# Kernel optimization log

Hardware: AMD Instinct MI355X
Metric: run time of the kernel (lower is better)

## Reference

```python
import jax, jax.numpy as jnp
import numpy as np

IMG = 1536
STRIDES = [8, 16, 32, 64, 128]
SCALES = np.array([2.0 ** 0, 2.0 ** (1.0 / 3.0), 2.0 ** (2.0 / 3.0)])
RATIOS = np.array([0.5, 1.0, 2.0])
THRESHOLD = 0.5
IOU_THRESHOLD = 0.5
N_KEEP = 1000  # fixed candidate budget for jit-compatible NMS


def make_anchors():
    """Multi-level RetinaNet-style anchors in (x1, y1, x2, y2), [A, 4]."""
    all_boxes = []
    for s in STRIDES:
        base = 4.0 * s
        fs = IMG // s
        areas = (base * SCALES) ** 2
        ws, hs = [], []
        for r in RATIOS:
            ws.append(np.sqrt(areas / r))
            hs.append(np.sqrt(areas * r))
        ws = np.concatenate(ws)  # [9]
        hs = np.concatenate(hs)
        cx = (np.arange(fs) + 0.5) * s
        cy = (np.arange(fs) + 0.5) * s
        cxg, cyg = np.meshgrid(cx, cy)
        cxg = cxg.reshape(-1, 1)
        cyg = cyg.reshape(-1, 1)
        boxes = np.stack([cxg - ws / 2, cyg - hs / 2, cxg + ws / 2, cyg + hs / 2], axis=-1)
        all_boxes.append(boxes.reshape(-1, 4))
    return np.concatenate(all_boxes, axis=0).astype(np.float32)


def setup_inputs() -> dict:
    key = jax.random.key(0)
    k1, k2 = jax.random.split(key)
    anchors = jnp.asarray(make_anchors())  # [441936, 4]
    A = anchors.shape[0]
    cla = jax.random.uniform(k1, (1, A, 80), dtype=jnp.float32)  # sigmoid-like class scores
    reg = 0.1 * jax.random.normal(k2, (1, A, 4), dtype=jnp.float32)  # box deltas
    return {"cla": cla, "reg": reg, "anchors": anchors, "height": IMG, "width": IMG}


def decode_box(anchors, deltas):
    wa = anchors[:, 2] - anchors[:, 0]
    ha = anchors[:, 3] - anchors[:, 1]
    cxa = anchors[:, 0] + 0.5 * wa
    cya = anchors[:, 1] + 0.5 * ha
    cx = cxa + deltas[:, 0] * wa
    cy = cya + deltas[:, 1] * ha
    w = wa * jnp.exp(deltas[:, 2])
    h = ha * jnp.exp(deltas[:, 3])
    return jnp.stack([cx - 0.5 * w, cy - 0.5 * h, cx + 0.5 * w, cy + 0.5 * h], axis=-1)


def iou_matrix(b):
    x1 = jnp.maximum(b[:, None, 0], b[None, :, 0])
    y1 = jnp.maximum(b[:, None, 1], b[None, :, 1])
    x2 = jnp.minimum(b[:, None, 2], b[None, :, 2])
    y2 = jnp.minimum(b[:, None, 3], b[None, :, 3])
    inter = jnp.clip(x2 - x1, 0.0) * jnp.clip(y2 - y1, 0.0)
    area = jnp.clip(b[:, 2] - b[:, 0], 0.0) * jnp.clip(b[:, 3] - b[:, 1], 0.0)
    union = area[:, None] + area[None, :] - inter
    return inter / jnp.maximum(union, 1e-8)


def reference(cla, reg, anchors, height, width):
    # decode + clip (clipbox)
    boxes = decode_box(anchors, reg[0])  # [A, 4]
    boxes = jnp.stack([
        jnp.clip(boxes[:, 0], 0.0, width - 1.0),
        jnp.clip(boxes[:, 1], 0.0, height - 1.0),
        jnp.clip(boxes[:, 2], 0.0, width - 1.0),
        jnp.clip(boxes[:, 3], 0.0, height - 1.0),
    ], axis=-1)
    # per-anchor best class score (torch.max over dim=2)
    scores_all = jnp.max(cla[0], axis=1)  # [A]
    # fixed-size candidate set replaces data-dependent boolean masking
    top_scores, idx = jax.lax.top_k(scores_all, N_KEEP)
    cand_boxes = boxes[idx]            # [N, 4]
    cand_cla = cla[0][idx]             # [N, C]
    valid = top_scores > THRESHOLD     # score thresholding
    iou = iou_matrix(cand_boxes)       # [N, N]

    def body(i, keep):
        suppressed = jnp.any(keep & (iou[i] > IOU_THRESHOLD))
        return keep.at[i].set(valid[i] & ~suppressed)

    keep = jax.lax.fori_loop(0, N_KEEP, body, jnp.zeros((N_KEEP,), dtype=bool))

    nms_scores = jnp.where(keep, jnp.max(cand_cla, axis=1), 0.0)
    nms_class = jnp.where(keep, jnp.argmax(cand_cla, axis=1), -1)
    nms_boxes = jnp.where(keep[:, None], cand_boxes, 0.0)
    return nms_scores, nms_class, nms_boxes
```

## Files before the change

### kernel.cpp

```cpp
#include <hip/hip_runtime.h>
#include <stdint.h>


#define NK 1000
#define CAP 2048
#define NCLS 80
#define NW 16
typedef unsigned long long ull;

static inline __device__ unsigned fkey(float f) {
  unsigned u = __float_as_uint(f);
  return (u & 0x80000000u) ? ~u : (u | 0x80000000u);
}
static inline __device__ float fkey_inv(unsigned k) {
  unsigned u = (k & 0x80000000u) ? (k & 0x7fffffffu) : ~k;
  return __uint_as_float(u);
}

__device__ __forceinline__ void scan_select(const unsigned* __restrict__ gh, int nbins,
                                            unsigned k, unsigned* s_sum, unsigned* s_res,
                                            unsigned& digit, unsigned& cum_above) {
  int t = threadIdx.x;
  int chunk = nbins >> 8;
  if (chunk < 1) chunk = 1;
  int base = t * chunk;
  unsigned s = 0;
  for (int b = 0; b < chunk; ++b) s += gh[base + b];
  s_sum[t] = s;
  __syncthreads();
  unsigned ca = 0;
  for (int u = t + 1; u < 256; ++u) ca += s_sum[u];
  if (ca < k && ca + s >= k) {
    unsigned cum = ca;
    for (int b = chunk - 1; b >= 0; --b) {
      unsigned c = gh[base + b];
      if (cum + c >= k) { s_res[0] = (unsigned)(base + b); s_res[1] = cum; break; }
      cum += c;
    }
  }
  __syncthreads();
  digit = s_res[0];
  cum_above = s_res[1];
  __syncthreads();
}

__global__ __launch_bounds__(256) void k_score(const float* __restrict__ cla,
                                               unsigned* __restrict__ keys,
                                               unsigned* __restrict__ hist0,
                                               uint4* __restrict__ zreg, int nz4,
                                               int A) {
  __shared__ unsigned lh[4096];
  int t = threadIdx.x;
  {
    const uint4 z = make_uint4(0u, 0u, 0u, 0u);
    int stride = gridDim.x * 256;
    for (int i = blockIdx.x * 256 + t; i < nz4; i += stride) zreg[i] = z;
  }
  for (int i = t; i < 4096; i += 256) lh[i] = 0u;
  __syncthreads();
  const int lane = t & 63, wib = t >> 6;
  const int gwave = blockIdx.x * 4 + wib, nwaves = gridDim.x * 4;
  const int q = lane >> 2, sub = lane & 3;
  const int ntask = (A + 15) >> 4;
  for (int task = gwave; task < ntask; task += nwaves) {
    int a = task * 16 + q;
    float m = -3.402823466e38f;
    if (a < A) {
      const float4* p = (const float4*)(cla + (size_t)a * NCLS);
#pragma unroll
      for (int j = 0; j < 5; ++j) {
        float4 v = p[sub + j * 4];
        m = fmaxf(m, fmaxf(fmaxf(v.x, v.y), fmaxf(v.z, v.w)));
      }
    }
    m = fmaxf(m, __shfl_xor(m, 1, 64));
    m = fmaxf(m, __shfl_xor(m, 2, 64));
    if (sub == 0 && a < A) {
      unsigned key = fkey(m);
      keys[a] = key;
      atomicAdd(&lh[key >> 20], 1u);
    }
  }
  __syncthreads();
  for (int i = t; i < 4096; i += 256) {
    unsigned c = lh[i];
    if (c) atomicAdd(&hist0[i], c);
  }
}

__global__ __launch_bounds__(256) void k_hist1(const unsigned* __restrict__ keys,
                                               const unsigned* __restrict__ hist0,
                                               unsigned* __restrict__ leaf,
                                               unsigned* __restrict__ summary, int A) {
  __shared__ unsigned lh[4096];
  __shared__ unsigned s_sum[256];
  __shared__ unsigned s_res[2];
  int t = threadIdx.x;
  unsigned d0, ca;
  scan_select(hist0, 4096, NK, s_sum, s_res, d0, ca);
  for (int i = t; i < 4096; i += 256) lh[i] = 0u;
  __syncthreads();
  int tid = blockIdx.x * 256 + t, nthr = gridDim.x * 256;
  for (int a = tid; a < A; a += nthr) {
    unsigned key = keys[a];
    if ((key >> 20) == d0) {
      unsigned low = key & 0xFFFFFu;
      atomicAdd(&leaf[low], 1u);
      atomicAdd(&lh[low >> 8], 1u);
    }
  }
  __syncthreads();
  for (int i = t; i < 4096; i += 256) {
    unsigned c = lh[i];
    if (c) atomicAdd(&summary[i], c);
  }
}

__global__ __launch_bounds__(256) void k_gather(const unsigned* __restrict__ keys,
                                                const unsigned* __restrict__ hist0,
                                                const unsigned* __restrict__ leaf,
                                                const unsigned* __restrict__ summary,
                                                unsigned* __restrict__ meta,
                                                ull* __restrict__ cand_keys, int A) {
  __shared__ unsigned s_sum[256];
  __shared__ unsigned s_res[2];
  __shared__ ull lbuf[1024];
  __shared__ unsigned lcnt;
  __shared__ unsigned gbase;
  int t = threadIdx.x;
  unsigned k_rem = NK, d0, g, b, ca;
  scan_select(hist0, 4096, k_rem, s_sum, s_res, d0, ca);
  k_rem -= ca;
  scan_select(summary, 4096, k_rem, s_sum, s_res, g, ca);
  k_rem -= ca;
  scan_select(leaf + (size_t)g * 256, 256, k_rem, s_sum, s_res, b, ca);
  const unsigned T = (d0 << 20) | (g << 8) | b;
  if (t == 0) lcnt = 0u;
  __syncthreads();
  int tid = blockIdx.x * 256 + t, nthr = gridDim.x * 256;
  for (int a = tid; a < A; a += nthr) {
    unsigned key = keys[a];
    if (key >= T) {
      unsigned pos = atomicAdd(&lcnt, 1u);
      if (pos < 1024)
        lbuf[pos] = ((ull)key << 32) | (ull)(~(unsigned)a);
    }
  }
  __syncthreads();
  if (t == 0) gbase = (lcnt > 0) ? atomicAdd(&meta[0], lcnt) : 0u;
  __syncthreads();
  unsigned n = lcnt < 1024u ? lcnt : 1024u;
  for (unsigned i = t; i < n; i += 256) {
    unsigned pos = gbase + i;
    if (pos < CAP) cand_keys[pos] = lbuf[i];
  }
}

__global__ __launch_bounds__(256) void k_rankdec(
    const float* __restrict__ cla, const float* __restrict__ reg,
    const float* __restrict__ anchors, const int* __restrict__ hp,
    const int* __restrict__ wp, const ull* __restrict__ cand_keys,
    float4* __restrict__ cand_box, float* __restrict__ cand_area,
    float* __restrict__ cand_score, int* __restrict__ cand_cls,
    int* __restrict__ cand_valid) {
  __shared__ ull skeys[CAP];
  int t = threadIdx.x;
  for (int i = t; i < CAP; i += 256) skeys[i] = cand_keys[i];
  __syncthreads();
  int c = blockIdx.x * 256 + t;
  ull ck = skeys[c];
  if (ck == 0ull) return;
  unsigned cnt = 0;
  const ulonglong2* sk2 = (const ulonglong2*)skeys;
#pragma unroll 4
  for (int j = 0; j < CAP / 2; ++j) {
    ulonglong2 v = sk2[j];
    cnt += (v.x > ck) ? 1u : 0u;
    cnt += (v.y > ck) ? 1u : 0u;
  }
  if (cnt >= NK) return;
  int rank = (int)cnt;
  unsigned a = ~(unsigned)(ck & 0xFFFFFFFFull);
  float score = fkey_inv((unsigned)(ck >> 32));
  float W1 = (float)wp[0] - 1.0f;
  float H1 = (float)hp[0] - 1.0f;
  float4 dd = ((const float4*)reg)[a];
  float4 an = ((const float4*)anchors)[a];
  float wa = an.z - an.x, ha = an.w - an.y;
  float cxa = an.x + 0.5f * wa, cya = an.y + 0.5f * ha;
  float cx = cxa + dd.x * wa, cy = cya + dd.y * ha;
  float w = wa * expf(dd.z), h = ha * expf(dd.w);
  float x1 = fminf(fmaxf(cx - 0.5f * w, 0.0f), W1);
  float y1 = fminf(fmaxf(cy - 0.5f * h, 0.0f), H1);
  float x2 = fminf(fmaxf(cx + 0.5f * w, 0.0f), W1);
  float y2 = fminf(fmaxf(cy + 0.5f * h, 0.0f), H1);
  cand_box[rank] = make_float4(x1, y1, x2, y2);
  cand_area[rank] = fmaxf(x2 - x1, 0.0f) * fmaxf(y2 - y1, 0.0f);
  cand_score[rank] = score;
  cand_valid[rank] = (score > 0.5f) ? 1 : 0;
  const float* row = cla + (size_t)a * NCLS;
  float m = -3.402823466e38f;
  int ci = 0;
#pragma unroll
  for (int j = 0; j < NCLS; ++j) {
    float v = row[j];
    if (v > m) { m = v; ci = j; }
  }
  cand_cls[rank] = ci;
}

__global__ __launch_bounds__(1024) void k_supres(const float4* __restrict__ cand_box,
                                                 const float* __restrict__ cand_area,
                                                 const int* __restrict__ cand_valid,
                                                 const float* __restrict__ cand_score,
                                                 const int* __restrict__ cand_cls,
                                                 ull* __restrict__ sup,
                                                 unsigned* __restrict__ meta,
                                                 float* __restrict__ out) {
  __shared__ float4 bx[NK];
  __shared__ float ar[NK];
  __shared__ unsigned keptm[32], notm[32];
  __shared__ int s_chg;
  __shared__ int s_last;
  int t = threadIdx.x;
  for (int i = t; i < NK; i += 1024) {
    bx[i] = cand_box[i];
    ar[i] = cand_area[i];
  }
  __syncthreads();
  {
    int gidx = blockIdx.x * 1024 + t;
    int i = gidx >> 4, w = gidx & 15;
    int j0 = w * 64;
    if (i < NK) {
      ull bits = 0ull;
      if (j0 <= i) {
        float4 bi = bx[i];
        float ai = ar[i];
#pragma unroll 4
        for (int s = 0; s < 64; ++s) {
          int jj = (s + w) & 63;
          int j = j0 + jj;
          if (j < NK) {
            float4 bj = bx[j];
            float xx1 = fmaxf(bi.x, bj.x), yy1 = fmaxf(bi.y, bj.y);
            float xx2 = fminf(bi.z, bj.z), yy2 = fminf(bi.w, bj.w);
            float inter = fmaxf(xx2 - xx1, 0.0f) * fmaxf(yy2 - yy1, 0.0f);
            float uni = ai + ar[j] - inter;
            float iou = inter / fmaxf(uni, 1e-8f);
            if (iou > 0.5f) bits |= (1ull << jj);
          }
        }
      }
      sup[(size_t)i * NW + w] = bits;
    }
  }
  __threadfence();
  __syncthreads();
  if (t == 0) {
    unsigned done = __hip_atomic_fetch_add(&meta[1], 1u, __ATOMIC_ACQ_REL,
                                           __HIP_MEMORY_SCOPE_AGENT);
    s_last = (done == gridDim.x - 1) ? 1 : 0;
    s_chg = 0;
  }
  __syncthreads();
  if (!s_last) return;
  if (t < 32) { keptm[t] = 0u; notm[t] = 0u; }
  int i = t;
  bool active = (i < NK);
  int wi = i >> 6;
  ull rw[NW];
  bool decided = true;
  if (active) {
#pragma unroll
    for (int w = 0; w < NW; ++w)
      rw[w] = __hip_atomic_load(&sup[(size_t)i * NW + w], __ATOMIC_RELAXED,
                                __HIP_MEMORY_SCOPE_AGENT);
    int bi = i & 63;
    ull dmask = (bi == 0) ? 0ull : ((1ull << bi) - 1ull);
#pragma unroll
    for (int w = 0; w < NW; ++w)
      rw[w] = (w < wi) ? rw[w] : ((w == wi) ? (rw[w] & dmask) : 0ull);
    decided = (cand_valid[i] == 0);
  }
  __syncthreads();
  if (active && decided) atomicOr(&notm[i >> 5], 1u << (i & 31));
  __syncthreads();
  for (int round = 0; round < NK; ++round) {
    if (active && !decided) {
      ull hit = 0ull, pot = 0ull;
#pragma unroll
      for (int w = 0; w < NW; ++w) {
        ull km = ((ull)keptm[2 * w + 1] << 32) | (ull)keptm[2 * w];
        ull nm = ((ull)notm[2 * w + 1] << 32) | (ull)notm[2 * w];
        hit |= rw[w] & km;
        pot |= rw[w] & ~(km | nm);
      }
      if (hit) {
        decided = true;
        atomicOr(&notm[i >> 5], 1u << (i & 31));
        s_chg = 1;
      } else if (!pot) {
        decided = true;
        atomicOr(&keptm[i >> 5], 1u << (i & 31));
        s_chg = 1;
      }
    }
    __syncthreads();
    if (s_chg == 0) break;
    __syncthreads();
    if (t == 0) s_chg = 0;
    __syncthreads();
  }
  for (int i2 = t; i2 < NK; i2 += 1024) {
    bool kp = (keptm[i2 >> 5] >> (i2 & 31)) & 1u;
    out[i2] = kp ? cand_score[i2] : 0.0f;
    out[NK + i2] = kp ? (float)cand_cls[i2] : -1.0f;
    float4 bo = bx[i2];
    ((float4*)(out + 2 * NK))[i2] = kp ? bo : make_float4(0.f, 0.f, 0.f, 0.f);
  }
}

extern "C" void kernel_launch(void* const* d_in, const int* in_sizes, int n_in,
                              void* d_out, int out_size, void* d_ws, size_t ws_size,
                              hipStream_t stream) {
  const float* cla = (const float*)d_in[0];
  const float* reg = (const float*)d_in[1];
  const float* anchors = (const float*)d_in[2];
  const int* hp = (const int*)d_in[3];
  const int* wp = (const int*)d_in[4];
  float* out = (float*)d_out;
  int A = in_sizes[2] / 4;

  char* ws = (char*)d_ws;
  size_t off = 0;
  auto carve = [&](size_t bytes) -> void* {
    void* p = ws + off;
    off += bytes;
    off = (off + 255) & ~(size_t)255;
    return p;
  };
  unsigned* keys = (unsigned*)carve((size_t)A * 4);
  unsigned* hist0 = (unsigned*)carve(4096 * 4);
  char* zbase = ws + off;
  unsigned* leaf = (unsigned*)carve((size_t)(1 << 20) * 4);
  unsigned* summary = (unsigned*)carve(4096 * 4);
  unsigned* meta = (unsigned*)carve(2 * 4);
  ull* cand_keys = (ull*)carve(CAP * 8);
  size_t zbytes = (size_t)((ws + off) - zbase);
  int nz4 = (int)(zbytes / 16);
  float4* cand_box = (float4*)carve(1024 * 16);
  float* cand_area = (float*)carve(1024 * 4);
  float* cand_score = (float*)carve(1024 * 4);
  int* cand_cls = (int*)carve(1024 * 4);
  int* cand_valid = (int*)carve(1024 * 4);
  ull* sup = (ull*)carve((size_t)1024 * NW * 8);
  (void)ws_size;
  (void)n_in;
  (void)out_size;

  hipMemsetAsync(hist0, 0, 4096 * 4, stream);
  k_score<<<1024, 256, 0, stream>>>(cla, keys, hist0, (uint4*)zbase, nz4, A);
  k_hist1<<<512, 256, 0, stream>>>(keys, hist0, leaf, summary, A);
  k_gather<<<512, 256, 0, stream>>>(keys, hist0, leaf, summary, meta, cand_keys, A);
  k_rankdec<<<8, 256, 0, stream>>>(cla, reg, anchors, hp, wp, cand_keys, cand_box,
                                   cand_area, cand_score, cand_cls, cand_valid);
  k_supres<<<16, 1024, 0, stream>>>(cand_box, cand_area, cand_valid, cand_score,
                                    cand_cls, sup, meta, out);
}
```

Baseline: 329.3 us.

## Fuse candidate ranking and box decode into the suppression kernel

Removes the separate rank/decode kernel and instead decodes each candidate box inside every suppression block, indexing candidates by their gather slot rather than their sorted rank. The IoU bitmask condition changes from an index comparison to a key comparison, so no prior sort is needed. Only the last block computes ranks, and it computes the argmax class only for kept boxes before scattering outputs to their rank positions. This saves one kernel launch and the global round-trip of the candidate arrays. In exchange the box decode is repeated across all 16 blocks and the suppression matrix is built over 1024 unsorted slots.

New measurement: 313.9 us. -4.7%, faster.

```diff
diff --git a/kernel.cpp b/kernel.cpp
--- a/kernel.cpp
+++ b/kernel.cpp
@@ -4,6 +4,7 @@
 
 #define NK 1000
 #define CAP 2048
+#define NS 1024
 #define NCLS 80
 #define NW 16
 typedef unsigned long long ull;
@@ -25,17 +26,20 @@
   if (chunk < 1) chunk = 1;
   int base = t * chunk;
   unsigned s = 0;
-  for (int b = 0; b < chunk; ++b) s += gh[base + b];
-  s_sum[t] = s;
-  __syncthreads();
-  unsigned ca = 0;
-  for (int u = t + 1; u < 256; ++u) ca += s_sum[u];
-  if (ca < k && ca + s >= k) {
-    unsigned cum = ca;
-    for (int b = chunk - 1; b >= 0; --b) {
-      unsigned c = gh[base + b];
-      if (cum + c >= k) { s_res[0] = (unsigned)(base + b); s_res[1] = cum; break; }
-      cum += c;
+  if (t < 256)
+    for (int b = 0; b < chunk; ++b) s += gh[base + b];
+  if (t < 256) s_sum[t] = s;
+  __syncthreads();
+  if (t < 256) {
+    unsigned ca = 0;
+    for (int u = t + 1; u < 256; ++u) ca += s_sum[u];
+    if (ca < k && ca + s >= k) {
+      unsigned cum = ca;
+      for (int b = chunk - 1; b >= 0; --b) {
+        unsigned c = gh[base + b];
+        if (cum + c >= k) { s_res[0] = (unsigned)(base + b); s_res[1] = cum; break; }
+        cum += c;
+      }
     }
   }
   __syncthreads();
@@ -156,104 +160,71 @@
   }
 }
 
-__global__ __launch_bounds__(256) void k_rankdec(
+__global__ __launch_bounds__(1024) void k_supdec(
     const float* __restrict__ cla, const float* __restrict__ reg,
     const float* __restrict__ anchors, const int* __restrict__ hp,
     const int* __restrict__ wp, const ull* __restrict__ cand_keys,
-    float4* __restrict__ cand_box, float* __restrict__ cand_area,
-    float* __restrict__ cand_score, int* __restrict__ cand_cls,
-    int* __restrict__ cand_valid) {
-  __shared__ ull skeys[CAP];
-  int t = threadIdx.x;
-  for (int i = t; i < CAP; i += 256) skeys[i] = cand_keys[i];
-  __syncthreads();
-  int c = blockIdx.x * 256 + t;
-  ull ck = skeys[c];
-  if (ck == 0ull) return;
-  unsigned cnt = 0;
-  const ulonglong2* sk2 = (const ulonglong2*)skeys;
-#pragma unroll 4
-  for (int j = 0; j < CAP / 2; ++j) {
-    ulonglong2 v = sk2[j];
-    cnt += (v.x > ck) ? 1u : 0u;
-    cnt += (v.y > ck) ? 1u : 0u;
-  }
-  if (cnt >= NK) return;
-  int rank = (int)cnt;
-  unsigned a = ~(unsigned)(ck & 0xFFFFFFFFull);
-  float score = fkey_inv((unsigned)(ck >> 32));
-  float W1 = (float)wp[0] - 1.0f;
-  float H1 = (float)hp[0] - 1.0f;
-  float4 dd = ((const float4*)reg)[a];
-  float4 an = ((const float4*)anchors)[a];
-  float wa = an.z - an.x, ha = an.w - an.y;
-  float cxa = an.x + 0.5f * wa, cya = an.y + 0.5f * ha;
-  float cx = cxa + dd.x * wa, cy = cya + dd.y * ha;
-  float w = wa * expf(dd.z), h = ha * expf(dd.w);
-  float x1 = fminf(fmaxf(cx - 0.5f * w, 0.0f), W1);
-  float y1 = fminf(fmaxf(cy - 0.5f * h, 0.0f), H1);
-  float x2 = fminf(fmaxf(cx + 0.5f * w, 0.0f), W1);
-  float y2 = fminf(fmaxf(cy + 0.5f * h, 0.0f), H1);
-  cand_box[rank] = make_float4(x1, y1, x2, y2);
-  cand_area[rank] = fmaxf(x2 - x1, 0.0f) * fmaxf(y2 - y1, 0.0f);
-  cand_score[rank] = score;
-  cand_valid[rank] = (score > 0.5f) ? 1 : 0;
-  const float* row = cla + (size_t)a * NCLS;
-  float m = -3.402823466e38f;
-  int ci = 0;
-#pragma unroll
-  for (int j = 0; j < NCLS; ++j) {
-    float v = row[j];
-    if (v > m) { m = v; ci = j; }
-  }
-  cand_cls[rank] = ci;
-}
-
-__global__ __launch_bounds__(1024) void k_supres(const float4* __restrict__ cand_box,
-                                                 const float* __restrict__ cand_area,
-                                                 const int* __restrict__ cand_valid,
-                                                 const float* __restrict__ cand_score,
-                                                 const int* __restrict__ cand_cls,
-                                                 ull* __restrict__ sup,
-                                                 unsigned* __restrict__ meta,
-                                                 float* __restrict__ out) {
-  __shared__ float4 bx[NK];
-  __shared__ float ar[NK];
+    ull* __restrict__ sup, unsigned* __restrict__ meta,
+    float* __restrict__ out) {
+  __shared__ ull ckl[NS];
+  __shared__ float4 bx[NS];
+  __shared__ float ar[NS];
   __shared__ unsigned keptm[32], notm[32];
   __shared__ int s_chg;
   __shared__ int s_last;
   int t = threadIdx.x;
-  for (int i = t; i < NK; i += 1024) {
-    bx[i] = cand_box[i];
-    ar[i] = cand_area[i];
+  ckl[t] = cand_keys[t];
+  __syncthreads();
+  ull ck = ckl[t];
+  float score = 0.0f;
+  bool valid = false;
+  if (ck != 0ull) {
+    unsigned a = ~(unsigned)(ck & 0xFFFFFFFFull);
+    score = fkey_inv((unsigned)(ck >> 32));
+    float W1 = (float)wp[0] - 1.0f;
+    float H1 = (float)hp[0] - 1.0f;
+    float4 dd = ((const float4*)reg)[a];
+    float4 an = ((const float4*)anchors)[a];
+    float wa = an.z - an.x, ha = an.w - an.y;
+    float cxa = an.x + 0.5f * wa, cya = an.y + 0.5f * ha;
+    float cx = cxa + dd.x * wa, cy = cya + dd.y * ha;
+    float w = wa * expf(dd.z), h = ha * expf(dd.w);
+    float x1 = fminf(fmaxf(cx - 0.5f * w, 0.0f), W1);
+    float y1 = fminf(fmaxf(cy - 0.5f * h, 0.0f), H1);
+    float x2 = fminf(fmaxf(cx + 0.5f * w, 0.0f), W1);
+    float y2 = fminf(fmaxf(cy + 0.5f * h, 0.0f), H1);
+    bx[t] = make_float4(x1, y1, x2, y2);
+    ar[t] = fmaxf(x2 - x1, 0.0f) * fmaxf(y2 - y1, 0.0f);
+    valid = (score > 0.5f);
+  } else {
+    bx[t] = make_float4(0.f, 0.f, 0.f, 0.f);
+    ar[t] = 0.0f;
   }
   __syncthreads();
   {
     int gidx = blockIdx.x * 1024 + t;
     int i = gidx >> 4, w = gidx & 15;
+    ull cki = ckl[i];
+    float4 bi = bx[i];
+    float ai = ar[i];
+    ull bits = 0ull;
     int j0 = w * 64;
-    if (i < NK) {
-      ull bits = 0ull;
-      if (j0 <= i) {
-        float4 bi = bx[i];
-        float ai = ar[i];
 #pragma unroll 4
-        for (int s = 0; s < 64; ++s) {
-          int jj = (s + w) & 63;
-          int j = j0 + jj;
-          if (j < NK) {
-            float4 bj = bx[j];
-            float xx1 = fmaxf(bi.x, bj.x), yy1 = fmaxf(bi.y, bj.y);
-            float xx2 = fminf(bi.z, bj.z), yy2 = fminf(bi.w, bj.w);
-            float inter = fmaxf(xx2 - xx1, 0.0f) * fmaxf(yy2 - yy1, 0.0f);
-            float uni = ai + ar[j] - inter;
-            float iou = inter / fmaxf(uni, 1e-8f);
-            if (iou > 0.5f) bits |= (1ull << jj);
-          }
-        }
-      }
-      sup[(size_t)i * NW + w] = bits;
-    }
+    for (int s = 0; s < 64; ++s) {
+      int jj = (s + w) & 63;
+      int j = j0 + jj;
+      ull ckj = ckl[j];
+      if (ckj > cki) {
+        float4 bj = bx[j];
+        float xx1 = fmaxf(bi.x, bj.x), yy1 = fmaxf(bi.y, bj.y);
+        float xx2 = fminf(bi.z, bj.z), yy2 = fminf(bi.w, bj.w);
+        float inter = fmaxf(xx2 - xx1, 0.0f) * fmaxf(yy2 - yy1, 0.0f);
+        float uni = ai + ar[j] - inter;
+        float iou = inter / fmaxf(uni, 1e-8f);
+        if (iou > 0.5f) bits |= (1ull << jj);
+      }
+    }
+    sup[(size_t)i * NW + w] = bits;
   }
   __threadfence();
   __syncthreads();
@@ -265,29 +236,21 @@
   }
   __syncthreads();
   if (!s_last) return;
+  unsigned rnk = 0;
+  for (int j = 0; j < NS; ++j) rnk += (ckl[j] > ck) ? 1u : 0u;
   if (t < 32) { keptm[t] = 0u; notm[t] = 0u; }
-  int i = t;
-  bool active = (i < NK);
-  int wi = i >> 6;
+  bool active = (ck != 0ull) && (rnk < NK);
+  bool decided = (!active) || (!valid);
   ull rw[NW];
-  bool decided = true;
-  if (active) {
 #pragma unroll
-    for (int w = 0; w < NW; ++w)
-      rw[w] = __hip_atomic_load(&sup[(size_t)i * NW + w], __ATOMIC_RELAXED,
-                                __HIP_MEMORY_SCOPE_AGENT);
-    int bi = i & 63;
-    ull dmask = (bi == 0) ? 0ull : ((1ull << bi) - 1ull);
-#pragma unroll
-    for (int w = 0; w < NW; ++w)
-      rw[w] = (w < wi) ? rw[w] : ((w == wi) ? (rw[w] & dmask) : 0ull);
-    decided = (cand_valid[i] == 0);
-  }
-  __syncthreads();
-  if (active && decided) atomicOr(&notm[i >> 5], 1u << (i & 31));
-  __syncthreads();
-  for (int round = 0; round < NK; ++round) {
-    if (active && !decided) {
+  for (int w = 0; w < NW; ++w)
+    rw[w] = __hip_atomic_load(&sup[(size_t)t * NW + w], __ATOMIC_RELAXED,
+                              __HIP_MEMORY_SCOPE_AGENT);
+  __syncthreads();
+  if (decided) atomicOr(&notm[t >> 5], 1u << (t & 31));
+  __syncthreads();
+  for (int round = 0; round < NS; ++round) {
+    if (!decided) {
       ull hit = 0ull, pot = 0ull;
 #pragma unroll
       for (int w = 0; w < NW; ++w) {
@@ -298,11 +261,11 @@
       }
       if (hit) {
         decided = true;
-        atomicOr(&notm[i >> 5], 1u << (i & 31));
+        atomicOr(&notm[t >> 5], 1u << (t & 31));
         s_chg = 1;
       } else if (!pot) {
         decided = true;
-        atomicOr(&keptm[i >> 5], 1u << (i & 31));
+        atomicOr(&keptm[t >> 5], 1u << (t & 31));
         s_chg = 1;
       }
     }
@@ -312,12 +275,23 @@
     if (t == 0) s_chg = 0;
     __syncthreads();
   }
-  for (int i2 = t; i2 < NK; i2 += 1024) {
-    bool kp = (keptm[i2 >> 5] >> (i2 & 31)) & 1u;
-    out[i2] = kp ? cand_score[i2] : 0.0f;
-    out[NK + i2] = kp ? (float)cand_cls[i2] : -1.0f;
-    float4 bo = bx[i2];
-    ((float4*)(out + 2 * NK))[i2] = kp ? bo : make_float4(0.f, 0.f, 0.f, 0.f);
+  if (active) {
+    bool kp = (keptm[t >> 5] >> (t & 31)) & 1u;
+    int ci = 0;
+    if (kp) {
+      unsigned a = ~(unsigned)(ck & 0xFFFFFFFFull);
+      const float* row = cla + (size_t)a * NCLS;
+      float m = -3.402823466e38f;
+#pragma unroll
+      for (int j = 0; j < NCLS; ++j) {
+        float v = row[j];
+        if (v > m) { m = v; ci = j; }
+      }
+    }
+    out[rnk] = kp ? score : 0.0f;
+    out[NK + rnk] = kp ? (float)ci : -1.0f;
+    float4 bo = bx[t];
+    ((float4*)(out + 2 * NK))[rnk] = kp ? bo : make_float4(0.f, 0.f, 0.f, 0.f);
   }
 }
 
@@ -349,12 +323,7 @@
   ull* cand_keys = (ull*)carve(CAP * 8);
   size_t zbytes = (size_t)((ws + off) - zbase);
   int nz4 = (int)(zbytes / 16);
-  float4* cand_box = (float4*)carve(1024 * 16);
-  float* cand_area = (float*)carve(1024 * 4);
-  float* cand_score = (float*)carve(1024 * 4);
-  int* cand_cls = (int*)carve(1024 * 4);
-  int* cand_valid = (int*)carve(1024 * 4);
-  ull* sup = (ull*)carve((size_t)1024 * NW * 8);
+  ull* sup = (ull*)carve((size_t)NS * NW * 8);
   (void)ws_size;
   (void)n_in;
   (void)out_size;
@@ -363,8 +332,6 @@
   k_score<<<1024, 256, 0, stream>>>(cla, keys, hist0, (uint4*)zbase, nz4, A);
   k_hist1<<<512, 256, 0, stream>>>(keys, hist0, leaf, summary, A);
   k_gather<<<512, 256, 0, stream>>>(keys, hist0, leaf, summary, meta, cand_keys, A);
-  k_rankdec<<<8, 256, 0, stream>>>(cla, reg, anchors, hp, wp, cand_keys, cand_box,
-                                   cand_area, cand_score, cand_cls, cand_valid);
-  k_supres<<<16, 1024, 0, stream>>>(cand_box, cand_area, cand_valid, cand_score,
-                                    cand_cls, sup, meta, out);
-}
+  k_supdec<<<16, 1024, 0, stream>>>(cla, reg, anchors, hp, wp, cand_keys, sup, meta,
+                                    out);
+}
```
